# Kernel tuning notes

Hardware: AMD Instinct MI355X
Metric: run time of the kernel (lower is better)

Reference implementation:

```python
import jax, jax.numpy as jnp
import numpy as np

TAU = 1.0      # gumbel-softmax temperature
ALPHA = 0.05   # mixprop alpha
GDEP = 1       # mixprop depth

B, C, H, W = 16, 512, 96, 96
N = 64  # n_classes / codebook size


def setup_inputs() -> dict:
    key = jax.random.key(0)
    ks = jax.random.split(key, 8)
    u = jax.random.uniform(ks[3], (B, N, H, W), dtype=jnp.float32, minval=1e-6, maxval=1.0 - 1e-6)
    gumbel_noise = -jnp.log(-jnp.log(u))  # standard Gumbel(0,1)
    return {
        "x": jax.random.normal(ks[0], (B, C, H, W), dtype=jnp.float32),
        "centers": jax.random.normal(ks[1], (N, C), dtype=jnp.float32) * 0.1,
        "A": jax.random.uniform(ks[2], (N, N), dtype=jnp.float32),
        "gumbel_noise": gumbel_noise,
        "W_bc": jax.random.normal(ks[4], (1, C), dtype=jnp.float32) * 0.05,
        "b_bc": jnp.zeros((1,), dtype=jnp.float32),
        "W_gcn": jax.random.normal(ks[5], (C, 2 * C), dtype=jnp.float32) * 0.03,
        "b_gcn": jnp.zeros((C,), dtype=jnp.float32),
    }


def _mixprop_centers(centers, A, W_gcn, b_gcn):
    # mixprop on the codebook: centers [N, C] viewed as x of shape [1, C, N, 1]
    n = A.shape[0]
    adj = A + jnp.eye(n, dtype=A.dtype)
    a = adj / adj.sum(axis=1, keepdims=True)           # row-normalized adjacency
    xg = centers.T[None, :, :, None]                    # [1, C, N, 1]
    h = xg
    outs = [h]
    for _ in range(GDEP):
        h = ALPHA * xg + (1.0 - ALPHA) * jnp.einsum('ncwl,vw->ncvl', h, a)
        outs.append(h)
    ho = jnp.concatenate(outs, axis=1)                  # [1, (GDEP+1)*C, N, 1]
    new_c = jnp.einsum('oc,bcvl->bovl', W_gcn, ho) + b_gcn[None, :, None, None]
    return new_c[0, :, :, 0].T                          # [N, C]


def reference(x, centers, A, gumbel_noise, W_bc, b_bc, W_gcn, b_gcn):
    n = centers.shape[0]
    # inner products of features with codebook centers
    inner_products = jnp.einsum('bchw,nc->bnhw', x, centers)          # [B, N, H, W]
    # gumbel-softmax with hard (straight-through) assignment over dim 1
    y = jax.nn.softmax((inner_products + gumbel_noise) / TAU, axis=1)
    hard = jax.nn.one_hot(jnp.argmax(y, axis=1), n, dtype=y.dtype, axis=1)
    one_hot = hard + y - jax.lax.stop_gradient(y)
    # quantized features via codebook gather
    z_q = jnp.einsum('bnhw,nd->bdhw', one_hot, centers)               # [B, C, H, W]
    # 1x1 conv binary classifier + global average pool
    heatmap = jnp.einsum('oc,bchw->bohw', W_bc, z_q) + b_bc[None, :, None, None]  # [B,1,H,W]
    logits = heatmap.mean(axis=(2, 3)).squeeze()                      # [B]
    # graph diffusion of the codebook
    new_centers = _mixprop_centers(centers, A, W_gcn, b_gcn)          # [N, C]
    normed_ip = jnp.einsum('bchw,nc->bnhw', x, new_centers)           # [B, N, H, W]
    cluster_probs = jax.nn.one_hot(jnp.argmax(normed_ip, axis=1), n, dtype=normed_ip.dtype, axis=1)
    cluster_loss = -(cluster_probs * jax.nn.softmax(normed_ip, axis=1)).sum(axis=1).mean()
    return heatmap, logits, cluster_loss, inner_products
```

## Files before the change

### kernel.cpp

```cpp
#include <hip/hip_runtime.h>
#include <math.h>

#define BATCH   16
#define CDIM    512
#define HWDIM   9216
#define NCLS    64
#define TILE    128
#define NTILES  72
#define NCHUNK  16

#define LOGOFF  147456
#define LOSSOFF 147472
#define IPOFF   147473

#define WS_CC   0
#define WS_S    65536
#define WS_PH   65600
#define WS_PC   66752
#define WS_AP   67904
#define WS_MIX  166208

typedef __attribute__((ext_vector_type(8))) short bf16x8;
typedef __attribute__((ext_vector_type(4))) float f32x4;

__device__ __forceinline__ void split3(float v, float& h, float& m, float& l) {
  float hf = __uint_as_float(__float_as_uint(v) & 0xFFFF0000u);
  float r  = v - hf;
  float mf = __uint_as_float(__float_as_uint(r) & 0xFFFF0000u);
  float r2 = r - mf;
  float lf = __uint_as_float(__float_as_uint(r2) & 0xFFFF0000u);
  h = hf; m = mf; l = lf;
}

__device__ __forceinline__ unsigned packbf(float a, float b) {
  return (__float_as_uint(a) >> 16) | (__float_as_uint(b) & 0xFFFF0000u);
}

__global__ __launch_bounds__(256) void prep1_kernel(
    const float* __restrict__ centers, const float* __restrict__ Aadj,
    const float* __restrict__ W_bc, const float* __restrict__ b_bc,
    float* __restrict__ ws) {
  __shared__ float a_n[NCLS];
  __shared__ float red[256];
  const int n = blockIdx.x;
  const int tid = threadIdx.x;

  if (tid < NCLS) a_n[tid] = Aadj[n * NCLS + tid] + (tid == n ? 1.0f : 0.0f);
  __syncthreads();
  if (tid == 0) {
    float ssum = 0.f;
    for (int w = 0; w < NCLS; ++w) ssum += a_n[w];
    red[0] = 1.0f / ssum;
  }
  __syncthreads();
  float inv = red[0];
  __syncthreads();
  if (tid < NCLS) a_n[tid] *= inv;
  __syncthreads();

  float p = 0.f;
  for (int c = tid; c < CDIM; c += 256) {
    float v = centers[n * CDIM + c];
    ws[WS_CC + n * CDIM + c] = v;
    float acc = 0.f;
    #pragma unroll 8
    for (int w = 0; w < NCLS; ++w) acc = fmaf(a_n[w], centers[w * CDIM + c], acc);
    ws[WS_MIX + n * CDIM + c] = 0.05f * v + 0.95f * acc;
    p = fmaf(W_bc[c], v, p);
  }
  red[tid] = p;
  __syncthreads();
  for (int st = 128; st > 0; st >>= 1) {
    if (tid < st) red[tid] += red[tid + st];
    __syncthreads();
  }
  if (tid == 0) ws[WS_S + n] = red[0] + b_bc[0];
}

__global__ __launch_bounds__(256) void prep2_kernel(
    const float* __restrict__ W_gcn, const float* __restrict__ b_gcn,
    float* __restrict__ ws) {
  __shared__ float catT[128][65];
  const int tid = threadIdx.x;
  const int oo = tid >> 6, n = tid & 63;
  const int o = blockIdx.x * 4 + oo;
  const float* Wrow = W_gcn + (size_t)o * 1024;
  float acc = b_gcn[o];

  for (int k0 = 0; k0 < 1024; k0 += 128) {
    __syncthreads();
    const float* srcb = (k0 < 512) ? (ws + WS_CC + k0) : (ws + WS_MIX + (k0 - 512));
    #pragma unroll
    for (int i = 0; i < 32; ++i) {
      int idx = i * 256 + tid;
      int kk = idx & 127, n2 = idx >> 7;
      catT[kk][n2] = srcb[(size_t)n2 * CDIM + kk];
    }
    __syncthreads();
    #pragma unroll 16
    for (int kk = 0; kk < 128; ++kk)
      acc = fmaf(Wrow[k0 + kk], catT[kk][n], acc);
  }
  ws[WS_CC + (size_t)(NCLS + n) * CDIM + o] = acc;
}

__global__ __launch_bounds__(256) void pack_kernel(float* __restrict__ ws) {
  const int gid = blockIdx.x * 256 + threadIdx.x;
  const int lane = gid & 63;
  const int mb = (gid >> 6) & 7;
  const int c = gid >> 9;
  const int row = mb * 16 + (lane & 15);
  const int kb = c * 32 + ((lane >> 4) & 3) * 8;
  const float* src = ws + WS_CC + (size_t)row * CDIM + kb;
  float e[8];
  *(float4*)&e[0] = *(const float4*)(src);
  *(float4*)&e[4] = *(const float4*)(src + 4);
  unsigned dh[4], dm[4], dl[4];
  #pragma unroll
  for (int d = 0; d < 4; ++d) {
    float h0, m0, l0, h1, m1, l1;
    split3(e[2 * d], h0, m0, l0);
    split3(e[2 * d + 1], h1, m1, l1);
    dh[d] = packbf(h0, h1); dm[d] = packbf(m0, m1); dl[d] = packbf(l0, l1);
  }
  const size_t base = WS_AP + (size_t)c * 6144 + (size_t)mb * 256 + (size_t)lane * 4;
  *(uint4*)(ws + base)        = make_uint4(dh[0], dh[1], dh[2], dh[3]);
  *(uint4*)(ws + base + 2048) = make_uint4(dm[0], dm[1], dm[2], dm[3]);
  *(uint4*)(ws + base + 4096) = make_uint4(dl[0], dl[1], dl[2], dl[3]);
}

__global__ __launch_bounds__(256, 3) void main_kernel(
    const float* __restrict__ x, const float* __restrict__ gumbel,
    float* __restrict__ ws, float* __restrict__ out) {
  __shared__ char ldsmem[49152];
  __shared__ float s_sh[NCLS];
  char* buf0 = ldsmem;
  char* buf1 = ldsmem + 24576;

  const int tid = threadIdx.x;
  const int w = tid >> 6, l = tid & 63;
  const int tile = blockIdx.x, b = blockIdx.y;
  const int hw0 = tile * TILE;

  if (tid < NCLS) s_sh[tid] = ws[WS_S + tid];

  const float* xb = x + (size_t)b * CDIM * HWDIM;
  const float* pB = xb + (size_t)(w * 8) * HWDIM + hw0 + l;
  const char* ap = (const char*)(ws + WS_AP);

  f32x4 cip[8], cnp[8];
  #pragma unroll
  for (int i = 0; i < 8; ++i) {
    cip[i] = (f32x4){0.f, 0.f, 0.f, 0.f};
    cnp[i] = (f32x4){0.f, 0.f, 0.f, 0.f};
  }

  float bre[16];
  bf16x8 A0[5], A1[5];
  const int la16 = l * 16;

#define LOAD_A(AS, c_) do {                                                   \
    const char* asrc = ap + (size_t)(c_) * 24576;                             \
    AS[0] = *(const bf16x8*)(asrc + w * 1024 + la16);                         \
    AS[1] = *(const bf16x8*)(asrc + 8192 + w * 1024 + la16);                  \
    AS[2] = *(const bf16x8*)(asrc + 16384 + w * 1024 + la16);                 \
    AS[3] = *(const bf16x8*)(asrc + (4 + w) * 1024 + la16);                   \
    AS[4] = *(const bf16x8*)(asrc + 8192 + (4 + w) * 1024 + la16);            \
  } while (0)

#define LOAD_B(c_) do {                                                       \
    const size_t koff = (size_t)(c_) * 32 * HWDIM;                            \
    _Pragma("unroll")                                                         \
    for (int j = 0; j < 8; ++j) {                                             \
      bre[j]     = pB[koff + (size_t)j * HWDIM];                              \
      bre[8 + j] = pB[koff + (size_t)j * HWDIM + 64];                         \
    }                                                                         \
  } while (0)

#define WRITE_B(WB) do {                                                      \
    _Pragma("unroll")                                                         \
    for (int hh = 0; hh < 2; ++hh) {                                          \
      unsigned dh[4], dm[4], dl[4];                                           \
      _Pragma("unroll")                                                       \
      for (int d = 0; d < 4; ++d) {                                           \
        float h0, m0, l0, h1, m1, l1;                                         \
        split3(bre[hh * 8 + 2 * d], h0, m0, l0);                              \
        split3(bre[hh * 8 + 2 * d + 1], h1, m1, l1);                          \
        dh[d] = packbf(h0, h1); dm[d] = packbf(m0, m1); dl[d] = packbf(l0, l1);\
      }                                                                       \
      char* basep = (WB) + ((((l >> 4) + hh * 4) * 64) + (w << 4) + (l & 15)) * 16; \
      *(uint4*)(basep)         = make_uint4(dh[0], dh[1], dh[2], dh[3]);      \
      *(uint4*)(basep + 8192)  = make_uint4(dm[0], dm[1], dm[2], dm[3]);      \
      *(uint4*)(basep + 16384) = make_uint4(dl[0], dl[1], dl[2], dl[3]);      \
    }                                                                         \
  } while (0)

#define CHUNK(c_, RB, WB, AC, AN) do {                                        \
    if ((c_) + 1 < NCHUNK) { LOAD_A(AN, (c_) + 1); LOAD_B((c_) + 1); }        \
    _Pragma("unroll")                                                         \
    for (int nb = 0; nb < 8; ++nb) {                                          \
      bf16x8 bH = *(const bf16x8*)((RB) + nb * 1024 + la16);                  \
      bf16x8 bM = *(const bf16x8*)((RB) + 8192 + nb * 1024 + la16);           \
      bf16x8 bL = *(const bf16x8*)((RB) + 16384 + nb * 1024 + la16);          \
      cip[nb] = __builtin_amdgcn_mfma_f32_16x16x32_bf16(AC[0], bH, cip[nb], 0, 0, 0); \
      cip[nb] = __builtin_amdgcn_mfma_f32_16x16x32_bf16(AC[0], bM, cip[nb], 0, 0, 0); \
      cip[nb] = __builtin_amdgcn_mfma_f32_16x16x32_bf16(AC[1], bH, cip[nb], 0, 0, 0); \
      cip[nb] = __builtin_amdgcn_mfma_f32_16x16x32_bf16(AC[0], bL, cip[nb], 0, 0, 0); \
      cip[nb] = __builtin_amdgcn_mfma_f32_16x16x32_bf16(AC[1], bM, cip[nb], 0, 0, 0); \
      cip[nb] = __builtin_amdgcn_mfma_f32_16x16x32_bf16(AC[2], bH, cip[nb], 0, 0, 0); \
      cnp[nb] = __builtin_amdgcn_mfma_f32_16x16x32_bf16(AC[3], bH, cnp[nb], 0, 0, 0); \
      cnp[nb] = __builtin_amdgcn_mfma_f32_16x16x32_bf16(AC[3], bM, cnp[nb], 0, 0, 0); \
      cnp[nb] = __builtin_amdgcn_mfma_f32_16x16x32_bf16(AC[4], bH, cnp[nb], 0, 0, 0); \
    }                                                                         \
    if ((c_) + 1 < NCHUNK) WRITE_B(WB);                                       \
    __syncthreads();                                                          \
  } while (0)

  LOAD_A(A0, 0);
  LOAD_B(0);
  WRITE_B(buf0);
  __syncthreads();

  for (int cc = 0; cc < NCHUNK; cc += 2) {
    CHUNK(cc, buf0, buf1, A0, A1);
    CHUNK(cc + 1, buf1, buf0, A1, A0);
  }

  float* pvv  = (float*)ldsmem;
  int*   pvi  = (int*)(ldsmem + 2048);
  float* pnm  = (float*)(ldsmem + 4096);
  float* pns  = (float*)(ldsmem + 6144);
  float* m2   = (float*)(ldsmem + 8192);
  float* hbuf = (float*)(ldsmem + 8704);
  float* cbuf = (float*)(ldsmem + 9216);

  const size_t bn = (size_t)b * NCLS;
  float* ipo = out + IPOFF;
  const int rbase = 16 * w + (l >> 4) * 4;
  const int c15 = l & 15;

  float bv[8]; int bi[8]; float nm[8];
  #pragma unroll
  for (int nb = 0; nb < 8; ++nb) {
    const int hw = hw0 + nb * 16 + c15;
    float best = -1e30f; int besti = 0;
    #pragma unroll
    for (int r = 0; r < 4; ++r) {
      const int n = rbase + r;
      const float v = cip[nb][r];
      ipo[(bn + n) * HWDIM + hw] = v;
      const float t = v + gumbel[(bn + n) * HWDIM + hw];
      if (t > best) { best = t; besti = n; }
    }
    bv[nb] = best; bi[nb] = besti;
    float m = cnp[nb][0];
    m = fmaxf(m, cnp[nb][1]); m = fmaxf(m, cnp[nb][2]); m = fmaxf(m, cnp[nb][3]);
    nm[nb] = m;
  }
  #pragma unroll
  for (int nb = 0; nb < 8; ++nb) {
    #pragma unroll
    for (int mk = 16; mk <= 32; mk <<= 1) {
      float ov = __shfl_xor(bv[nb], mk);
      int   oi = __shfl_xor(bi[nb], mk);
      if (ov > bv[nb] || (ov == bv[nb] && oi < bi[nb])) { bv[nb] = ov; bi[nb] = oi; }
      nm[nb] = fmaxf(nm[nb], __shfl_xor(nm[nb], mk));
    }
  }
  if ((l >> 4) == 0) {
    #pragma unroll
    for (int nb = 0; nb < 8; ++nb) {
      pvv[w * 128 + nb * 16 + l] = bv[nb];
      pvi[w * 128 + nb * 16 + l] = bi[nb];
      pnm[w * 128 + nb * 16 + l] = nm[nb];
    }
  }
  __syncthreads();

  if (tid < 128) {
    float v = pvv[tid]; int i = pvi[tid];
    #pragma unroll
    for (int ww = 1; ww < 4; ++ww) {
      float v2 = pvv[ww * 128 + tid]; int i2 = pvi[ww * 128 + tid];
      if (v2 > v || (v2 == v && i2 < i)) { v = v2; i = i2; }
    }
    float h = s_sh[i];
    hbuf[tid] = h;
    out[(size_t)b * HWDIM + hw0 + tid] = h;
    float m = pnm[tid];
    #pragma unroll
    for (int ww = 1; ww < 4; ++ww) m = fmaxf(m, pnm[ww * 128 + tid]);
    m2[tid] = m;
  }
  __syncthreads();

  #pragma unroll
  for (int nb = 0; nb < 8; ++nb) {
    const float mm = m2[nb * 16 + c15];
    float s = __expf(cnp[nb][0] - mm) + __expf(cnp[nb][1] - mm)
            + __expf(cnp[nb][2] - mm) + __expf(cnp[nb][3] - mm);
    s += __shfl_xor(s, 16);
    s += __shfl_xor(s, 32);
    if ((l >> 4) == 0) pns[w * 128 + nb * 16 + l] = s;
  }
  __syncthreads();

  if (tid < 128) {
    float S = pns[tid] + pns[128 + tid] + pns[256 + tid] + pns[384 + tid];
    cbuf[tid] = 1.0f / S;
  }
  __syncthreads();

  if (tid < 64) {
    float hs = hbuf[tid] + hbuf[tid + 64];
    float cs = cbuf[tid] + cbuf[tid + 64];
    #pragma unroll
    for (int o = 32; o > 0; o >>= 1) {
      hs += __shfl_down(hs, o);
      cs += __shfl_down(cs, o);
    }
    if (tid == 0) {
      ws[WS_PH + b * NTILES + tile] = hs;
      ws[WS_PC + b * NTILES + tile] = cs;
    }
  }
#undef LOAD_A
#undef LOAD_B
#undef WRITE_B
#undef CHUNK
}

__global__ __launch_bounds__(256) void finish_kernel(
    const float* __restrict__ ws, float* __restrict__ out) {
  __shared__ double sred[256];
  const int tid = threadIdx.x;
  {
    int bb = tid >> 4, lane = tid & 15;
    double s = 0.0;
    for (int t = lane; t < NTILES; t += 16) s += (double)ws[WS_PH + bb * NTILES + t];
    #pragma unroll
    for (int o = 8; o > 0; o >>= 1) s += __shfl_down(s, o, 16);
    if (lane == 0) out[LOGOFF + bb] = (float)(s / (double)HWDIM);
  }
  double c = 0.0;
  for (int i = tid; i < BATCH * NTILES; i += 256) c += (double)ws[WS_PC + i];
  sred[tid] = c;
  __syncthreads();
  for (int st = 128; st > 0; st >>= 1) {
    if (tid < st) sred[tid] += sred[tid + st];
    __syncthreads();
  }
  if (tid == 0) out[LOSSOFF] = (float)(-sred[0] / (double)(BATCH * HWDIM));
}

extern "C" void kernel_launch(void* const* d_in, const int* in_sizes, int n_in,
                              void* d_out, int out_size, void* d_ws, size_t ws_size,
                              hipStream_t stream) {
  const float* x       = (const float*)d_in[0];
  const float* centers = (const float*)d_in[1];
  const float* Aadj    = (const float*)d_in[2];
  const float* gumbel  = (const float*)d_in[3];
  const float* W_bc    = (const float*)d_in[4];
  const float* b_bc    = (const float*)d_in[5];
  const float* W_gcn   = (const float*)d_in[6];
  const float* b_gcn   = (const float*)d_in[7];
  float* out = (float*)d_out;
  float* ws  = (float*)d_ws;

  hipLaunchKernelGGL(prep1_kernel, dim3(NCLS), dim3(256), 0, stream,
                     centers, Aadj, W_bc, b_bc, ws);
  hipLaunchKernelGGL(prep2_kernel, dim3(128), dim3(256), 0, stream,
                     W_gcn, b_gcn, ws);
  hipLaunchKernelGGL(pack_kernel, dim3(32), dim3(256), 0, stream, ws);
  hipLaunchKernelGGL(main_kernel, dim3(NTILES, BATCH), dim3(256), 0, stream,
                     x, gumbel, ws, out);
  hipLaunchKernelGGL(finish_kernel, dim3(1), dim3(256), 0, stream, ws, out);
}
```

Baseline: 206.3 us.

## Keep x fragments in registers per wave and drop the LDS staging

Each wave now owns 32 spatial columns across all 64 classes. It loads its x slice straight from global memory into registers, double-buffered, and splits it into bf16 fragments in place, so the LDS buffers and the per-chunk barriers go away. The codebook A-fragments are read from global or L2 inside every phase instead of being prefetched. Argmax and softmax reductions now finish within a wave, leaving one barrier at the end. The cost is fewer lanes per x load (16-wide coalescing), more repeated A traffic, and higher register pressure, with occupancy dropped to 2 blocks.

```diff
diff --git a/kernel.cpp b/kernel.cpp
--- a/kernel.cpp
+++ b/kernel.cpp
@@ -22,6 +22,7 @@
 
 typedef __attribute__((ext_vector_type(8))) short bf16x8;
 typedef __attribute__((ext_vector_type(4))) float f32x4;
+typedef __attribute__((ext_vector_type(4))) unsigned int u32x4;
 
 __device__ __forceinline__ void split3(float v, float& h, float& m, float& l) {
   float hf = __uint_as_float(__float_as_uint(v) & 0xFFFF0000u);
@@ -129,205 +130,165 @@
   *(uint4*)(ws + base + 4096) = make_uint4(dl[0], dl[1], dl[2], dl[3]);
 }
 
-__global__ __launch_bounds__(256, 3) void main_kernel(
+__global__ __launch_bounds__(256, 2) void main_kernel(
     const float* __restrict__ x, const float* __restrict__ gumbel,
     float* __restrict__ ws, float* __restrict__ out) {
-  __shared__ char ldsmem[49152];
-  __shared__ float s_sh[NCLS];
-  char* buf0 = ldsmem;
-  char* buf1 = ldsmem + 24576;
+  __shared__ float redH[4];
+  __shared__ float redC[4];
 
   const int tid = threadIdx.x;
   const int w = tid >> 6, l = tid & 63;
+  const int q = l >> 4, c15 = l & 15;
   const int tile = blockIdx.x, b = blockIdx.y;
   const int hw0 = tile * TILE;
-
-  if (tid < NCLS) s_sh[tid] = ws[WS_S + tid];
+  const int jw = hw0 + w * 32;
 
   const float* xb = x + (size_t)b * CDIM * HWDIM;
-  const float* pB = xb + (size_t)(w * 8) * HWDIM + hw0 + l;
+  const float* pB = xb + (size_t)q * 8 * HWDIM + jw + c15;
   const char* ap = (const char*)(ws + WS_AP);
-
-  f32x4 cip[8], cnp[8];
+  const int la16 = l * 16;
+
+  f32x4 cip[4][2], cnp[4][2];
   #pragma unroll
-  for (int i = 0; i < 8; ++i) {
-    cip[i] = (f32x4){0.f, 0.f, 0.f, 0.f};
-    cnp[i] = (f32x4){0.f, 0.f, 0.f, 0.f};
-  }
-
-  float bre[16];
-  bf16x8 A0[5], A1[5];
-  const int la16 = l * 16;
-
-#define LOAD_A(AS, c_) do {                                                   \
-    const char* asrc = ap + (size_t)(c_) * 24576;                             \
-    AS[0] = *(const bf16x8*)(asrc + w * 1024 + la16);                         \
-    AS[1] = *(const bf16x8*)(asrc + 8192 + w * 1024 + la16);                  \
-    AS[2] = *(const bf16x8*)(asrc + 16384 + w * 1024 + la16);                 \
-    AS[3] = *(const bf16x8*)(asrc + (4 + w) * 1024 + la16);                   \
-    AS[4] = *(const bf16x8*)(asrc + 8192 + (4 + w) * 1024 + la16);            \
-  } while (0)
-
-#define LOAD_B(c_) do {                                                       \
-    const size_t koff = (size_t)(c_) * 32 * HWDIM;                            \
+  for (int mb = 0; mb < 4; ++mb)
+    #pragma unroll
+    for (int nb = 0; nb < 2; ++nb) {
+      cip[mb][nb] = (f32x4){0.f, 0.f, 0.f, 0.f};
+      cnp[mb][nb] = (f32x4){0.f, 0.f, 0.f, 0.f};
+    }
+
+  float br0[16], br1[16];
+  bf16x8 fH[2], fM[2], fL[2];
+
+#define LOADB(BR, c_) do {                                                    \
     _Pragma("unroll")                                                         \
-    for (int j = 0; j < 8; ++j) {                                             \
-      bre[j]     = pB[koff + (size_t)j * HWDIM];                              \
-      bre[8 + j] = pB[koff + (size_t)j * HWDIM + 64];                         \
+    for (int e = 0; e < 8; ++e) {                                             \
+      BR[e * 2 + 0] = pB[(size_t)((c_) * 32 + e) * HWDIM];                    \
+      BR[e * 2 + 1] = pB[(size_t)((c_) * 32 + e) * HWDIM + 16];               \
     }                                                                         \
   } while (0)
 
-#define WRITE_B(WB) do {                                                      \
+#define SPLITB(BR) do {                                                      \
     _Pragma("unroll")                                                         \
-    for (int hh = 0; hh < 2; ++hh) {                                          \
-      unsigned dh[4], dm[4], dl[4];                                           \
+    for (int nb = 0; nb < 2; ++nb) {                                          \
+      u32x4 vh, vm, vl;                                                       \
       _Pragma("unroll")                                                       \
       for (int d = 0; d < 4; ++d) {                                           \
         float h0, m0, l0, h1, m1, l1;                                         \
-        split3(bre[hh * 8 + 2 * d], h0, m0, l0);                              \
-        split3(bre[hh * 8 + 2 * d + 1], h1, m1, l1);                          \
-        dh[d] = packbf(h0, h1); dm[d] = packbf(m0, m1); dl[d] = packbf(l0, l1);\
+        split3(BR[(2 * d) * 2 + nb], h0, m0, l0);                             \
+        split3(BR[(2 * d + 1) * 2 + nb], h1, m1, l1);                         \
+        vh[d] = packbf(h0, h1); vm[d] = packbf(m0, m1); vl[d] = packbf(l0, l1);\
       }                                                                       \
-      char* basep = (WB) + ((((l >> 4) + hh * 4) * 64) + (w << 4) + (l & 15)) * 16; \
-      *(uint4*)(basep)         = make_uint4(dh[0], dh[1], dh[2], dh[3]);      \
-      *(uint4*)(basep + 8192)  = make_uint4(dm[0], dm[1], dm[2], dm[3]);      \
-      *(uint4*)(basep + 16384) = make_uint4(dl[0], dl[1], dl[2], dl[3]);      \
+      fH[nb] = __builtin_bit_cast(bf16x8, vh);                                \
+      fM[nb] = __builtin_bit_cast(bf16x8, vm);                                \
+      fL[nb] = __builtin_bit_cast(bf16x8, vl);                                \
     }                                                                         \
   } while (0)
 
-#define CHUNK(c_, RB, WB, AC, AN) do {                                        \
-    if ((c_) + 1 < NCHUNK) { LOAD_A(AN, (c_) + 1); LOAD_B((c_) + 1); }        \
+#define PHASE(c_) do {                                                        \
+    const char* asrc = ap + (size_t)(c_) * 24576;                             \
     _Pragma("unroll")                                                         \
-    for (int nb = 0; nb < 8; ++nb) {                                          \
-      bf16x8 bH = *(const bf16x8*)((RB) + nb * 1024 + la16);                  \
-      bf16x8 bM = *(const bf16x8*)((RB) + 8192 + nb * 1024 + la16);           \
-      bf16x8 bL = *(const bf16x8*)((RB) + 16384 + nb * 1024 + la16);          \
-      cip[nb] = __builtin_amdgcn_mfma_f32_16x16x32_bf16(AC[0], bH, cip[nb], 0, 0, 0); \
-      cip[nb] = __builtin_amdgcn_mfma_f32_16x16x32_bf16(AC[0], bM, cip[nb], 0, 0, 0); \
-      cip[nb] = __builtin_amdgcn_mfma_f32_16x16x32_bf16(AC[1], bH, cip[nb], 0, 0, 0); \
-      cip[nb] = __builtin_amdgcn_mfma_f32_16x16x32_bf16(AC[0], bL, cip[nb], 0, 0, 0); \
-      cip[nb] = __builtin_amdgcn_mfma_f32_16x16x32_bf16(AC[1], bM, cip[nb], 0, 0, 0); \
-      cip[nb] = __builtin_amdgcn_mfma_f32_16x16x32_bf16(AC[2], bH, cip[nb], 0, 0, 0); \
-      cnp[nb] = __builtin_amdgcn_mfma_f32_16x16x32_bf16(AC[3], bH, cnp[nb], 0, 0, 0); \
-      cnp[nb] = __builtin_amdgcn_mfma_f32_16x16x32_bf16(AC[3], bM, cnp[nb], 0, 0, 0); \
-      cnp[nb] = __builtin_amdgcn_mfma_f32_16x16x32_bf16(AC[4], bH, cnp[nb], 0, 0, 0); \
+    for (int mb = 0; mb < 4; ++mb) {                                          \
+      bf16x8 aH = *(const bf16x8*)(asrc + mb * 1024 + la16);                  \
+      bf16x8 aM = *(const bf16x8*)(asrc + 8192 + mb * 1024 + la16);           \
+      bf16x8 aL = *(const bf16x8*)(asrc + 16384 + mb * 1024 + la16);          \
+      _Pragma("unroll")                                                       \
+      for (int nb = 0; nb < 2; ++nb) {                                        \
+        cip[mb][nb] = __builtin_amdgcn_mfma_f32_16x16x32_bf16(aH, fH[nb], cip[mb][nb], 0, 0, 0); \
+        cip[mb][nb] = __builtin_amdgcn_mfma_f32_16x16x32_bf16(aH, fM[nb], cip[mb][nb], 0, 0, 0); \
+        cip[mb][nb] = __builtin_amdgcn_mfma_f32_16x16x32_bf16(aM, fH[nb], cip[mb][nb], 0, 0, 0); \
+        cip[mb][nb] = __builtin_amdgcn_mfma_f32_16x16x32_bf16(aH, fL[nb], cip[mb][nb], 0, 0, 0); \
+        cip[mb][nb] = __builtin_amdgcn_mfma_f32_16x16x32_bf16(aM, fM[nb], cip[mb][nb], 0, 0, 0); \
+        cip[mb][nb] = __builtin_amdgcn_mfma_f32_16x16x32_bf16(aL, fH[nb], cip[mb][nb], 0, 0, 0); \
+      }                                                                       \
     }                                                                         \
-    if ((c_) + 1 < NCHUNK) WRITE_B(WB);                                       \
-    __syncthreads();                                                          \
+    _Pragma("unroll")                                                         \
+    for (int mb = 0; mb < 4; ++mb) {                                          \
+      bf16x8 nH = *(const bf16x8*)(asrc + (4 + mb) * 1024 + la16);            \
+      bf16x8 nM = *(const bf16x8*)(asrc + 8192 + (4 + mb) * 1024 + la16);     \
+      _Pragma("unroll")                                                       \
+      for (int nb = 0; nb < 2; ++nb) {                                        \
+        cnp[mb][nb] = __builtin_amdgcn_mfma_f32_16x16x32_bf16(nH, fH[nb], cnp[mb][nb], 0, 0, 0); \
+        cnp[mb][nb] = __builtin_amdgcn_mfma_f32_16x16x32_bf16(nH, fM[nb], cnp[mb][nb], 0, 0, 0); \
+        cnp[mb][nb] = __builtin_amdgcn_mfma_f32_16x16x32_bf16(nM, fH[nb], cnp[mb][nb], 0, 0, 0); \
+      }                                                                       \
+    }                                                                         \
   } while (0)
 
-  LOAD_A(A0, 0);
-  LOAD_B(0);
-  WRITE_B(buf0);
-  __syncthreads();
-
-  for (int cc = 0; cc < NCHUNK; cc += 2) {
-    CHUNK(cc, buf0, buf1, A0, A1);
-    CHUNK(cc + 1, buf1, buf0, A1, A0);
-  }
-
-  float* pvv  = (float*)ldsmem;
-  int*   pvi  = (int*)(ldsmem + 2048);
-  float* pnm  = (float*)(ldsmem + 4096);
-  float* pns  = (float*)(ldsmem + 6144);
-  float* m2   = (float*)(ldsmem + 8192);
-  float* hbuf = (float*)(ldsmem + 8704);
-  float* cbuf = (float*)(ldsmem + 9216);
+  LOADB(br0, 0);
+  LOADB(br1, 1);
+  #pragma unroll 1
+  for (int c = 0; c < NCHUNK; c += 2) {
+    SPLITB(br0);
+    if (c + 2 < NCHUNK) LOADB(br0, c + 2);
+    PHASE(c);
+    SPLITB(br1);
+    if (c + 3 < NCHUNK) LOADB(br1, c + 3);
+    PHASE(c + 1);
+  }
 
   const size_t bn = (size_t)b * NCLS;
   float* ipo = out + IPOFF;
-  const int rbase = 16 * w + (l >> 4) * 4;
-  const int c15 = l & 15;
-
-  float bv[8]; int bi[8]; float nm[8];
+  float hcol[2], scol[2];
+
   #pragma unroll
-  for (int nb = 0; nb < 8; ++nb) {
-    const int hw = hw0 + nb * 16 + c15;
-    float best = -1e30f; int besti = 0;
-    #pragma unroll
-    for (int r = 0; r < 4; ++r) {
-      const int n = rbase + r;
-      const float v = cip[nb][r];
-      ipo[(bn + n) * HWDIM + hw] = v;
-      const float t = v + gumbel[(bn + n) * HWDIM + hw];
-      if (t > best) { best = t; besti = n; }
+  for (int nb = 0; nb < 2; ++nb) {
+    const int col = jw + nb * 16 + c15;
+    float best = -1e30f; int bi = 0;
+    #pragma unroll
+    for (int mb = 0; mb < 4; ++mb) {
+      #pragma unroll
+      for (int r = 0; r < 4; ++r) {
+        const int m = mb * 16 + q * 4 + r;
+        const size_t off = (bn + m) * HWDIM + col;
+        const float v = cip[mb][nb][r];
+        ipo[off] = v;
+        const float t = v + gumbel[off];
+        if (t > best) { best = t; bi = m; }
+      }
     }
-    bv[nb] = best; bi[nb] = besti;
-    float m = cnp[nb][0];
-    m = fmaxf(m, cnp[nb][1]); m = fmaxf(m, cnp[nb][2]); m = fmaxf(m, cnp[nb][3]);
-    nm[nb] = m;
-  }
+    #pragma unroll
+    for (int mk = 16; mk <= 32; mk <<= 1) {
+      float ov = __shfl_xor(best, mk);
+      int   oi = __shfl_xor(bi, mk);
+      if (ov > best || (ov == best && oi < bi)) { best = ov; bi = oi; }
+    }
+    hcol[nb] = ws[WS_S + bi];
+    if (q == 0) out[(size_t)b * HWDIM + col] = hcol[nb];
+
+    float mx = -1e30f;
+    #pragma unroll
+    for (int mb = 0; mb < 4; ++mb)
+      #pragma unroll
+      for (int r = 0; r < 4; ++r) mx = fmaxf(mx, cnp[mb][nb][r]);
+    #pragma unroll
+    for (int mk = 16; mk <= 32; mk <<= 1) mx = fmaxf(mx, __shfl_xor(mx, mk));
+    float se = 0.f;
+    #pragma unroll
+    for (int mb = 0; mb < 4; ++mb)
+      #pragma unroll
+      for (int r = 0; r < 4; ++r) se += __expf(cnp[mb][nb][r] - mx);
+    se += __shfl_xor(se, 16);
+    se += __shfl_xor(se, 32);
+    scol[nb] = 1.0f / se;
+  }
+
+  float ph = (q == 0) ? (hcol[0] + hcol[1]) : 0.f;
+  float pc = (q == 0) ? (scol[0] + scol[1]) : 0.f;
   #pragma unroll
-  for (int nb = 0; nb < 8; ++nb) {
-    #pragma unroll
-    for (int mk = 16; mk <= 32; mk <<= 1) {
-      float ov = __shfl_xor(bv[nb], mk);
-      int   oi = __shfl_xor(bi[nb], mk);
-      if (ov > bv[nb] || (ov == bv[nb] && oi < bi[nb])) { bv[nb] = ov; bi[nb] = oi; }
-      nm[nb] = fmaxf(nm[nb], __shfl_xor(nm[nb], mk));
-    }
-  }
-  if ((l >> 4) == 0) {
-    #pragma unroll
-    for (int nb = 0; nb < 8; ++nb) {
-      pvv[w * 128 + nb * 16 + l] = bv[nb];
-      pvi[w * 128 + nb * 16 + l] = bi[nb];
-      pnm[w * 128 + nb * 16 + l] = nm[nb];
-    }
-  }
-  __syncthreads();
-
-  if (tid < 128) {
-    float v = pvv[tid]; int i = pvi[tid];
-    #pragma unroll
-    for (int ww = 1; ww < 4; ++ww) {
-      float v2 = pvv[ww * 128 + tid]; int i2 = pvi[ww * 128 + tid];
-      if (v2 > v || (v2 == v && i2 < i)) { v = v2; i = i2; }
-    }
-    float h = s_sh[i];
-    hbuf[tid] = h;
-    out[(size_t)b * HWDIM + hw0 + tid] = h;
-    float m = pnm[tid];
-    #pragma unroll
-    for (int ww = 1; ww < 4; ++ww) m = fmaxf(m, pnm[ww * 128 + tid]);
-    m2[tid] = m;
-  }
-  __syncthreads();
-
-  #pragma unroll
-  for (int nb = 0; nb < 8; ++nb) {
-    const float mm = m2[nb * 16 + c15];
-    float s = __expf(cnp[nb][0] - mm) + __expf(cnp[nb][1] - mm)
-            + __expf(cnp[nb][2] - mm) + __expf(cnp[nb][3] - mm);
-    s += __shfl_xor(s, 16);
-    s += __shfl_xor(s, 32);
-    if ((l >> 4) == 0) pns[w * 128 + nb * 16 + l] = s;
-  }
-  __syncthreads();
-
-  if (tid < 128) {
-    float S = pns[tid] + pns[128 + tid] + pns[256 + tid] + pns[384 + tid];
-    cbuf[tid] = 1.0f / S;
-  }
-  __syncthreads();
-
-  if (tid < 64) {
-    float hs = hbuf[tid] + hbuf[tid + 64];
-    float cs = cbuf[tid] + cbuf[tid + 64];
-    #pragma unroll
-    for (int o = 32; o > 0; o >>= 1) {
-      hs += __shfl_down(hs, o);
-      cs += __shfl_down(cs, o);
-    }
-    if (tid == 0) {
-      ws[WS_PH + b * NTILES + tile] = hs;
-      ws[WS_PC + b * NTILES + tile] = cs;
-    }
-  }
-#undef LOAD_A
-#undef LOAD_B
-#undef WRITE_B
-#undef CHUNK
+  for (int o = 32; o > 0; o >>= 1) {
+    ph += __shfl_down(ph, o);
+    pc += __shfl_down(pc, o);
+  }
+  if (l == 0) { redH[w] = ph; redC[w] = pc; }
+  __syncthreads();
+  if (tid == 0) {
+    ws[WS_PH + b * NTILES + tile] = redH[0] + redH[1] + redH[2] + redH[3];
+    ws[WS_PC + b * NTILES + tile] = redC[0] + redC[1] + redC[2] + redC[3];
+  }
+#undef LOADB
+#undef SPLITB
+#undef PHASE
 }
 
 __global__ __launch_bounds__(256) void finish_kernel(
```

Measured after the change: 266.2 us. 29.1% more time.

## Deepen global-load prefetch to two chunks and use lighter LDS barriers

Applied to the files above, without the earlier changes.

Restructures the main GEMM loop so x tiles are prefetched two chunks ahead into two register sets (br0/br1), keeping more global loads in flight while MFMA runs. The A-operand (codebook split) fragments are now loaded just before use instead of being double-buffered in registers. __syncthreads is replaced by an explicit lgkmcnt(0) wait plus s_barrier, so the barrier no longer waits on outstanding global (vmcnt) loads. This raises register pressure from the extra 16-float buffer and exposes A-load latency at each phase start, which could hurt occupancy under the 3-blocks launch bound.

```diff
diff --git a/kernel.cpp b/kernel.cpp
--- a/kernel.cpp
+++ b/kernel.cpp
@@ -147,6 +147,7 @@
   const float* xb = x + (size_t)b * CDIM * HWDIM;
   const float* pB = xb + (size_t)(w * 8) * HWDIM + hw0 + l;
   const char* ap = (const char*)(ws + WS_AP);
+  const int la16 = l * 16;
 
   f32x4 cip[8], cnp[8];
   #pragma unroll
@@ -155,37 +156,26 @@
     cnp[i] = (f32x4){0.f, 0.f, 0.f, 0.f};
   }
 
-  float bre[16];
-  bf16x8 A0[5], A1[5];
-  const int la16 = l * 16;
-
-#define LOAD_A(AS, c_) do {                                                   \
-    const char* asrc = ap + (size_t)(c_) * 24576;                             \
-    AS[0] = *(const bf16x8*)(asrc + w * 1024 + la16);                         \
-    AS[1] = *(const bf16x8*)(asrc + 8192 + w * 1024 + la16);                  \
-    AS[2] = *(const bf16x8*)(asrc + 16384 + w * 1024 + la16);                 \
-    AS[3] = *(const bf16x8*)(asrc + (4 + w) * 1024 + la16);                   \
-    AS[4] = *(const bf16x8*)(asrc + 8192 + (4 + w) * 1024 + la16);            \
-  } while (0)
-
-#define LOAD_B(c_) do {                                                       \
+  float br0[16], br1[16];
+
+#define LOADB(BR, c_) do {                                                    \
     const size_t koff = (size_t)(c_) * 32 * HWDIM;                            \
     _Pragma("unroll")                                                         \
     for (int j = 0; j < 8; ++j) {                                             \
-      bre[j]     = pB[koff + (size_t)j * HWDIM];                              \
-      bre[8 + j] = pB[koff + (size_t)j * HWDIM + 64];                         \
+      BR[j]     = pB[koff + (size_t)j * HWDIM];                               \
+      BR[8 + j] = pB[koff + (size_t)j * HWDIM + 64];                          \
     }                                                                         \
   } while (0)
 
-#define WRITE_B(WB) do {                                                      \
+#define WRITE_B(WB, BR) do {                                                  \
     _Pragma("unroll")                                                         \
     for (int hh = 0; hh < 2; ++hh) {                                          \
       unsigned dh[4], dm[4], dl[4];                                           \
       _Pragma("unroll")                                                       \
       for (int d = 0; d < 4; ++d) {                                           \
         float h0, m0, l0, h1, m1, l1;                                         \
-        split3(bre[hh * 8 + 2 * d], h0, m0, l0);                              \
-        split3(bre[hh * 8 + 2 * d + 1], h1, m1, l1);                          \
+        split3(BR[hh * 8 + 2 * d], h0, m0, l0);                               \
+        split3(BR[hh * 8 + 2 * d + 1], h1, m1, l1);                           \
         dh[d] = packbf(h0, h1); dm[d] = packbf(m0, m1); dl[d] = packbf(l0, l1);\
       }                                                                       \
       char* basep = (WB) + ((((l >> 4) + hh * 4) * 64) + (w << 4) + (l & 15)) * 16; \
@@ -195,35 +185,53 @@
     }                                                                         \
   } while (0)
 
-#define CHUNK(c_, RB, WB, AC, AN) do {                                        \
-    if ((c_) + 1 < NCHUNK) { LOAD_A(AN, (c_) + 1); LOAD_B((c_) + 1); }        \
+#define PHASE(c_, RB) do {                                                    \
+    const char* asrc = ap + (size_t)(c_) * 24576;                             \
+    bf16x8 aH = *(const bf16x8*)(asrc + w * 1024 + la16);                     \
+    bf16x8 aM = *(const bf16x8*)(asrc + 8192 + w * 1024 + la16);              \
+    bf16x8 aL = *(const bf16x8*)(asrc + 16384 + w * 1024 + la16);             \
+    bf16x8 nH = *(const bf16x8*)(asrc + (4 + w) * 1024 + la16);               \
+    bf16x8 nM = *(const bf16x8*)(asrc + 8192 + (4 + w) * 1024 + la16);        \
     _Pragma("unroll")                                                         \
     for (int nb = 0; nb < 8; ++nb) {                                          \
       bf16x8 bH = *(const bf16x8*)((RB) + nb * 1024 + la16);                  \
       bf16x8 bM = *(const bf16x8*)((RB) + 8192 + nb * 1024 + la16);           \
       bf16x8 bL = *(const bf16x8*)((RB) + 16384 + nb * 1024 + la16);          \
-      cip[nb] = __builtin_amdgcn_mfma_f32_16x16x32_bf16(AC[0], bH, cip[nb], 0, 0, 0); \
-      cip[nb] = __builtin_amdgcn_mfma_f32_16x16x32_bf16(AC[0], bM, cip[nb], 0, 0, 0); \
-      cip[nb] = __builtin_amdgcn_mfma_f32_16x16x32_bf16(AC[1], bH, cip[nb], 0, 0, 0); \
-      cip[nb] = __builtin_amdgcn_mfma_f32_16x16x32_bf16(AC[0], bL, cip[nb], 0, 0, 0); \
-      cip[nb] = __builtin_amdgcn_mfma_f32_16x16x32_bf16(AC[1], bM, cip[nb], 0, 0, 0); \
-      cip[nb] = __builtin_amdgcn_mfma_f32_16x16x32_bf16(AC[2], bH, cip[nb], 0, 0, 0); \
-      cnp[nb] = __builtin_amdgcn_mfma_f32_16x16x32_bf16(AC[3], bH, cnp[nb], 0, 0, 0); \
-      cnp[nb] = __builtin_amdgcn_mfma_f32_16x16x32_bf16(AC[3], bM, cnp[nb], 0, 0, 0); \
-      cnp[nb] = __builtin_amdgcn_mfma_f32_16x16x32_bf16(AC[4], bH, cnp[nb], 0, 0, 0); \
+      cip[nb] = __builtin_amdgcn_mfma_f32_16x16x32_bf16(aH, bH, cip[nb], 0, 0, 0); \
+      cip[nb] = __builtin_amdgcn_mfma_f32_16x16x32_bf16(aH, bM, cip[nb], 0, 0, 0); \
+      cip[nb] = __builtin_amdgcn_mfma_f32_16x16x32_bf16(aM, bH, cip[nb], 0, 0, 0); \
+      cip[nb] = __builtin_amdgcn_mfma_f32_16x16x32_bf16(aH, bL, cip[nb], 0, 0, 0); \
+      cip[nb] = __builtin_amdgcn_mfma_f32_16x16x32_bf16(aM, bM, cip[nb], 0, 0, 0); \
+      cip[nb] = __builtin_amdgcn_mfma_f32_16x16x32_bf16(aL, bH, cip[nb], 0, 0, 0); \
+      cnp[nb] = __builtin_amdgcn_mfma_f32_16x16x32_bf16(nH, bH, cnp[nb], 0, 0, 0); \
+      cnp[nb] = __builtin_amdgcn_mfma_f32_16x16x32_bf16(nH, bM, cnp[nb], 0, 0, 0); \
+      cnp[nb] = __builtin_amdgcn_mfma_f32_16x16x32_bf16(nM, bH, cnp[nb], 0, 0, 0); \
     }                                                                         \
-    if ((c_) + 1 < NCHUNK) WRITE_B(WB);                                       \
-    __syncthreads();                                                          \
   } while (0)
 
-  LOAD_A(A0, 0);
-  LOAD_B(0);
-  WRITE_B(buf0);
-  __syncthreads();
-
-  for (int cc = 0; cc < NCHUNK; cc += 2) {
-    CHUNK(cc, buf0, buf1, A0, A1);
-    CHUNK(cc + 1, buf1, buf0, A1, A0);
+#define LGKM0_BARRIER() do {                                                  \
+    asm volatile("s_waitcnt lgkmcnt(0)" ::: "memory");                        \
+    __builtin_amdgcn_s_barrier();                                             \
+  } while (0)
+
+  LOADB(br0, 0);
+  LOADB(br1, 1);
+  WRITE_B(buf0, br0);
+  LOADB(br0, 2);
+  LGKM0_BARRIER();
+
+  #pragma unroll 1
+  for (int c = 0; c < NCHUNK; c += 2) {
+    PHASE(c, buf0);
+    WRITE_B(buf1, br1);
+    if (c + 3 < NCHUNK) LOADB(br1, c + 3);
+    LGKM0_BARRIER();
+    PHASE(c + 1, buf1);
+    if (c + 2 < NCHUNK) {
+      WRITE_B(buf0, br0);
+      if (c + 4 < NCHUNK) LOADB(br0, c + 4);
+    }
+    LGKM0_BARRIER();
   }
 
   float* pvv  = (float*)ldsmem;
@@ -236,7 +244,7 @@
 
   const size_t bn = (size_t)b * NCLS;
   float* ipo = out + IPOFF;
-  const int rbase = 16 * w + (l >> 4) * 4;
+  const int rbase = 16 * w + ((l >> 4) & 3) * 4;
   const int c15 = l & 15;
 
   float bv[8]; int bi[8]; float nm[8];
@@ -324,10 +332,10 @@
       ws[WS_PC + b * NTILES + tile] = cs;
     }
   }
-#undef LOAD_A
-#undef LOAD_B
+#undef LOADB
 #undef WRITE_B
-#undef CHUNK
+#undef PHASE
+#undef LGKM0_BARRIER
 }
 
 __global__ __launch_bounds__(256) void finish_kernel(
```

After: 222.9 us. 1.08x slower.

## Fuse prep kernels into one and fold final reduction into main kernel

Applied to the files above, without the earlier changes.

Merges the three small preprocessing kernels (mixprop, GCN projection, bf16 split packing) into one per-class kernel that keeps rows in shared memory. The final logits/loss reduction moves into the main kernel's last block, which an atomic counter with threadfences picks out. This cuts kernel launches and workspace round-trips. In exchange, each prep block reads all of W_gcn redundantly (64x), and correctness now depends on the counter being reset inside the prep kernel.

```diff
diff --git a/kernel.cpp b/kernel.cpp
--- a/kernel.cpp
+++ b/kernel.cpp
@@ -8,6 +8,7 @@
 #define TILE    128
 #define NTILES  72
 #define NCHUNK  16
+#define NBLOCKS (NTILES * BATCH)
 
 #define LOGOFF  147456
 #define LOSSOFF 147472
@@ -19,6 +20,7 @@
 #define WS_PC   66752
 #define WS_AP   67904
 #define WS_MIX  166208
+#define WS_CNT  198976
 
 typedef __attribute__((ext_vector_type(8))) short bf16x8;
 typedef __attribute__((ext_vector_type(4))) float f32x4;
@@ -36,15 +38,21 @@
   return (__float_as_uint(a) >> 16) | (__float_as_uint(b) & 0xFFFF0000u);
 }
 
-__global__ __launch_bounds__(256) void prep1_kernel(
+__global__ __launch_bounds__(256) void prep_kernel(
     const float* __restrict__ centers, const float* __restrict__ Aadj,
     const float* __restrict__ W_bc, const float* __restrict__ b_bc,
+    const float* __restrict__ W_gcn, const float* __restrict__ b_gcn,
     float* __restrict__ ws) {
+  __shared__ float c_row[CDIM];
+  __shared__ float mix_row[CDIM];
+  __shared__ float new_row[CDIM];
   __shared__ float a_n[NCLS];
   __shared__ float red[256];
   const int n = blockIdx.x;
   const int tid = threadIdx.x;
 
+  if (n == 0 && tid == 0) ((unsigned int*)ws)[WS_CNT] = 0u;
+
   if (tid < NCLS) a_n[tid] = Aadj[n * NCLS + tid] + (tid == n ? 1.0f : 0.0f);
   __syncthreads();
   if (tid == 0) {
@@ -61,11 +69,11 @@
   float p = 0.f;
   for (int c = tid; c < CDIM; c += 256) {
     float v = centers[n * CDIM + c];
-    ws[WS_CC + n * CDIM + c] = v;
+    c_row[c] = v;
     float acc = 0.f;
     #pragma unroll 8
     for (int w = 0; w < NCLS; ++w) acc = fmaf(a_n[w], centers[w * CDIM + c], acc);
-    ws[WS_MIX + n * CDIM + c] = 0.05f * v + 0.95f * acc;
+    mix_row[c] = 0.05f * v + 0.95f * acc;
     p = fmaf(W_bc[c], v, p);
   }
   red[tid] = p;
@@ -75,58 +83,57 @@
     __syncthreads();
   }
   if (tid == 0) ws[WS_S + n] = red[0] + b_bc[0];
-}
-
-__global__ __launch_bounds__(256) void prep2_kernel(
-    const float* __restrict__ W_gcn, const float* __restrict__ b_gcn,
-    float* __restrict__ ws) {
-  __shared__ float catT[128][65];
-  const int tid = threadIdx.x;
-  const int oo = tid >> 6, n = tid & 63;
-  const int o = blockIdx.x * 4 + oo;
-  const float* Wrow = W_gcn + (size_t)o * 1024;
-  float acc = b_gcn[o];
-
-  for (int k0 = 0; k0 < 1024; k0 += 128) {
-    __syncthreads();
-    const float* srcb = (k0 < 512) ? (ws + WS_CC + k0) : (ws + WS_MIX + (k0 - 512));
-    #pragma unroll
-    for (int i = 0; i < 32; ++i) {
-      int idx = i * 256 + tid;
-      int kk = idx & 127, n2 = idx >> 7;
-      catT[kk][n2] = srcb[(size_t)n2 * CDIM + kk];
-    }
-    __syncthreads();
-    #pragma unroll 16
-    for (int kk = 0; kk < 128; ++kk)
-      acc = fmaf(Wrow[k0 + kk], catT[kk][n], acc);
-  }
-  ws[WS_CC + (size_t)(NCLS + n) * CDIM + o] = acc;
-}
-
-__global__ __launch_bounds__(256) void pack_kernel(float* __restrict__ ws) {
-  const int gid = blockIdx.x * 256 + threadIdx.x;
-  const int lane = gid & 63;
-  const int mb = (gid >> 6) & 7;
-  const int c = gid >> 9;
-  const int row = mb * 16 + (lane & 15);
-  const int kb = c * 32 + ((lane >> 4) & 3) * 8;
-  const float* src = ws + WS_CC + (size_t)row * CDIM + kb;
-  float e[8];
-  *(float4*)&e[0] = *(const float4*)(src);
-  *(float4*)&e[4] = *(const float4*)(src + 4);
-  unsigned dh[4], dm[4], dl[4];
-  #pragma unroll
-  for (int d = 0; d < 4; ++d) {
-    float h0, m0, l0, h1, m1, l1;
-    split3(e[2 * d], h0, m0, l0);
-    split3(e[2 * d + 1], h1, m1, l1);
-    dh[d] = packbf(h0, h1); dm[d] = packbf(m0, m1); dl[d] = packbf(l0, l1);
-  }
-  const size_t base = WS_AP + (size_t)c * 6144 + (size_t)mb * 256 + (size_t)lane * 4;
-  *(uint4*)(ws + base)        = make_uint4(dh[0], dh[1], dh[2], dh[3]);
-  *(uint4*)(ws + base + 2048) = make_uint4(dm[0], dm[1], dm[2], dm[3]);
-  *(uint4*)(ws + base + 4096) = make_uint4(dl[0], dl[1], dl[2], dl[3]);
+  __syncthreads();
+
+  for (int o = tid; o < CDIM; o += 256) {
+    const float4* wr0 = (const float4*)(W_gcn + (size_t)o * 1024);
+    const float4* wr1 = (const float4*)(W_gcn + (size_t)o * 1024 + 512);
+    const float4* cr4 = (const float4*)c_row;
+    const float4* mr4 = (const float4*)mix_row;
+    float a0 = b_gcn[o], a1 = 0.f, a2 = 0.f, a3 = 0.f;
+    #pragma unroll 4
+    for (int qk = 0; qk < 128; ++qk) {
+      float4 wv = wr0[qk], cv = cr4[qk];
+      a0 = fmaf(wv.x, cv.x, a0);
+      a1 = fmaf(wv.y, cv.y, a1);
+      a2 = fmaf(wv.z, cv.z, a2);
+      a3 = fmaf(wv.w, cv.w, a3);
+    }
+    #pragma unroll 4
+    for (int qk = 0; qk < 128; ++qk) {
+      float4 wv = wr1[qk], mv = mr4[qk];
+      a0 = fmaf(wv.x, mv.x, a0);
+      a1 = fmaf(wv.y, mv.y, a1);
+      a2 = fmaf(wv.z, mv.z, a2);
+      a3 = fmaf(wv.w, mv.w, a3);
+    }
+    new_row[o] = (a0 + a1) + (a2 + a3);
+  }
+  __syncthreads();
+
+  if (tid < 128) {
+    const int rowsel = tid >> 6;
+    const int u = tid & 63;
+    const int c = u >> 2, q = u & 3;
+    const float* rbuf = rowsel ? new_row : c_row;
+    const int mb = (rowsel ? 4 : 0) + (n >> 4);
+    const int lane = q * 16 + (n & 15);
+    float e[8];
+    #pragma unroll
+    for (int i = 0; i < 8; ++i) e[i] = rbuf[c * 32 + q * 8 + i];
+    unsigned dh[4], dm[4], dl[4];
+    #pragma unroll
+    for (int d = 0; d < 4; ++d) {
+      float h0, m0, l0, h1, m1, l1;
+      split3(e[2 * d], h0, m0, l0);
+      split3(e[2 * d + 1], h1, m1, l1);
+      dh[d] = packbf(h0, h1); dm[d] = packbf(m0, m1); dl[d] = packbf(l0, l1);
+    }
+    float* dst = ws + WS_AP + (size_t)c * 6144 + (size_t)mb * 256 + (size_t)lane * 4;
+    *(uint4*)(dst)        = make_uint4(dh[0], dh[1], dh[2], dh[3]);
+    *(uint4*)(dst + 2048) = make_uint4(dm[0], dm[1], dm[2], dm[3]);
+    *(uint4*)(dst + 4096) = make_uint4(dl[0], dl[1], dl[2], dl[3]);
+  }
 }
 
 __global__ __launch_bounds__(256, 3) void main_kernel(
@@ -134,6 +141,7 @@
     float* __restrict__ ws, float* __restrict__ out) {
   __shared__ char ldsmem[49152];
   __shared__ float s_sh[NCLS];
+  __shared__ int lastflag;
   char* buf0 = ldsmem;
   char* buf1 = ldsmem + 24576;
 
@@ -147,6 +155,7 @@
   const float* xb = x + (size_t)b * CDIM * HWDIM;
   const float* pB = xb + (size_t)(w * 8) * HWDIM + hw0 + l;
   const char* ap = (const char*)(ws + WS_AP);
+  const int la16 = l * 16;
 
   f32x4 cip[8], cnp[8];
   #pragma unroll
@@ -157,7 +166,6 @@
 
   float bre[16];
   bf16x8 A0[5], A1[5];
-  const int la16 = l * 16;
 
 #define LOAD_A(AS, c_) do {                                                   \
     const char* asrc = ap + (size_t)(c_) * 24576;                             \
@@ -221,6 +229,7 @@
   WRITE_B(buf0);
   __syncthreads();
 
+  #pragma unroll 1
   for (int cc = 0; cc < NCHUNK; cc += 2) {
     CHUNK(cc, buf0, buf1, A0, A1);
     CHUNK(cc + 1, buf1, buf0, A1, A0);
@@ -236,7 +245,7 @@
 
   const size_t bn = (size_t)b * NCLS;
   float* ipo = out + IPOFF;
-  const int rbase = 16 * w + (l >> 4) * 4;
+  const int rbase = 16 * w + ((l >> 4) & 3) * 4;
   const int c15 = l & 15;
 
   float bv[8]; int bi[8]; float nm[8];
@@ -324,33 +333,38 @@
       ws[WS_PC + b * NTILES + tile] = cs;
     }
   }
+
+  __threadfence();
+  if (tid == 0) {
+    unsigned old = atomicAdd((unsigned int*)ws + WS_CNT, 1u);
+    lastflag = (old == (unsigned)(NBLOCKS - 1));
+  }
+  __syncthreads();
+  if (!lastflag) return;
+  __threadfence();
+
+  double* sred = (double*)ldsmem;
+  {
+    int bb = tid >> 4, lane = tid & 15;
+    double s = 0.0;
+    for (int t = lane; t < NTILES; t += 16) s += (double)ws[WS_PH + bb * NTILES + t];
+    #pragma unroll
+    for (int o = 8; o > 0; o >>= 1) s += __shfl_down(s, o, 16);
+    if (lane == 0) out[LOGOFF + bb] = (float)(s / (double)HWDIM);
+  }
+  double c = 0.0;
+  for (int i = tid; i < NBLOCKS; i += 256) c += (double)ws[WS_PC + i];
+  sred[tid] = c;
+  __syncthreads();
+  for (int st = 128; st > 0; st >>= 1) {
+    if (tid < st) sred[tid] += sred[tid + st];
+    __syncthreads();
+  }
+  if (tid == 0) out[LOSSOFF] = (float)(-sred[0] / (double)(BATCH * HWDIM));
 #undef LOAD_A
 #undef LOAD_B
 #undef WRITE_B
 #undef CHUNK
-}
-
-__global__ __launch_bounds__(256) void finish_kernel(
-    const float* __restrict__ ws, float* __restrict__ out) {
-  __shared__ double sred[256];
-  const int tid = threadIdx.x;
-  {
-    int bb = tid >> 4, lane = tid & 15;
-    double s = 0.0;
-    for (int t = lane; t < NTILES; t += 16) s += (double)ws[WS_PH + bb * NTILES + t];
-    #pragma unroll
-    for (int o = 8; o > 0; o >>= 1) s += __shfl_down(s, o, 16);
-    if (lane == 0) out[LOGOFF + bb] = (float)(s / (double)HWDIM);
-  }
-  double c = 0.0;
-  for (int i = tid; i < BATCH * NTILES; i += 256) c += (double)ws[WS_PC + i];
-  sred[tid] = c;
-  __syncthreads();
-  for (int st = 128; st > 0; st >>= 1) {
-    if (tid < st) sred[tid] += sred[tid + st];
-    __syncthreads();
-  }
-  if (tid == 0) out[LOSSOFF] = (float)(-sred[0] / (double)(BATCH * HWDIM));
 }
 
 extern "C" void kernel_launch(void* const* d_in, const int* in_sizes, int n_in,
@@ -367,12 +381,8 @@
   float* out = (float*)d_out;
   float* ws  = (float*)d_ws;
 
-  hipLaunchKernelGGL(prep1_kernel, dim3(NCLS), dim3(256), 0, stream,
-                     centers, Aadj, W_bc, b_bc, ws);
-  hipLaunchKernelGGL(prep2_kernel, dim3(128), dim3(256), 0, stream,
-                     W_gcn, b_gcn, ws);
-  hipLaunchKernelGGL(pack_kernel, dim3(32), dim3(256), 0, stream, ws);
+  hipLaunchKernelGGL(prep_kernel, dim3(NCLS), dim3(256), 0, stream,
+                     centers, Aadj, W_bc, b_bc, W_gcn, b_gcn, ws);
   hipLaunchKernelGGL(main_kernel, dim3(NTILES, BATCH), dim3(256), 0, stream,
                      x, gumbel, ws, out);
-  hipLaunchKernelGGL(finish_kernel, dim3(1), dim3(256), 0, stream, ws, out);
-}
+}
```

After: 372.5 us. 1.81x slower.
